# Performance work log

Hardware: AMD Instinct MI355X
Metric: run time of the kernel (lower is better)

The kernel has to match this reference:

```python
import jax, jax.numpy as jnp
import numpy as np
import math

B, S, D = 4, 2048, 1024
H, DH = 16, 64  # num_heads, head dim (hardcoded 64 in module)


def setup_inputs() -> dict:
    key = jax.random.key(0)
    ks = jax.random.split(key, 5)
    scale = 0.02
    return {
        "x": jax.random.normal(ks[0], (B, S, D), dtype=jnp.float32),
        "W_Q": jax.random.normal(ks[1], (D, H * DH), dtype=jnp.float32) * scale,
        "W_K": jax.random.normal(ks[2], (D, H * DH), dtype=jnp.float32) * scale,
        "W_V": jax.random.normal(ks[3], (D, H * DH), dtype=jnp.float32) * scale,
        "W_O": jax.random.normal(ks[4], (H * DH, D), dtype=jnp.float32) * scale,
        "ln_gamma": jnp.ones((D,), dtype=jnp.float32),
        "ln_beta": jnp.zeros((D,), dtype=jnp.float32),
    }


def reference(x, W_Q, W_K, W_V, W_O, ln_gamma, ln_beta):
    # QKV projections (bias=False Linear: x @ W)
    q = (x @ W_Q).reshape(B, S, H, DH).transpose(0, 2, 1, 3)  # [B,H,S,DH]
    k = (x @ W_K).reshape(B, S, H, DH).transpose(0, 2, 1, 3)
    v = (x @ W_V).reshape(B, S, H, DH).transpose(0, 2, 1, 3)

    # scaled scores with causal mask (upper triangle, diag=1 -> -1e7)
    scores = jnp.einsum("bhsd,bhtd->bhst", q, k) / math.sqrt(DH)  # [B,H,S,S]
    causal = jnp.triu(jnp.ones((S, S), dtype=bool), k=1)
    scores = jnp.where(causal, jnp.float32(-1e7), scores)
    attn = jax.nn.softmax(scores, axis=-1)
    ctx = jnp.einsum("bhst,bhtd->bhsd", attn, v)  # [B,H,S,DH]

    # merge heads, output proj, residual, LayerNorm
    out = ctx.transpose(0, 2, 1, 3).reshape(B, S, H * DH) @ W_O + x
    mu = jnp.mean(out, axis=-1, keepdims=True)
    var = jnp.mean((out - mu) ** 2, axis=-1, keepdims=True)
    out = (out - mu) * jax.lax.rsqrt(var + 1e-5) * ln_gamma + ln_beta
    return out
```

## Files before the change

kernel.cpp:

```cpp
#include <hip/hip_runtime.h>
#include <hip/hip_bf16.h>
#include <cstdint>
#include <cstddef>

#define S_ 2048
#define D_ 1024
#define H_ 16
#define DH_ 64
#define M_ 8192

using bf16 = __bf16;
using bf16x4 = __attribute__((ext_vector_type(4))) __bf16;
using bf16x8 = __attribute__((ext_vector_type(8))) __bf16;
using f32x4 = __attribute__((ext_vector_type(4))) float;
using s16x4 = __attribute__((ext_vector_type(4))) short;

__device__ __forceinline__ void g2lds16(const bf16* g, bf16* l) {
  __builtin_amdgcn_global_load_lds(
      (const __attribute__((address_space(1))) void*)g,
      (__attribute__((address_space(3))) void*)l, 16, 0, 0);
}

__device__ __forceinline__ f32x4 mfma16(bf16x4 a, bf16x4 b, f32x4 c) {
#if __has_builtin(__builtin_amdgcn_mfma_f32_16x16x16_bf16)
  return __builtin_amdgcn_mfma_f32_16x16x16_bf16(a, b, c, 0, 0, 0);
#elif __has_builtin(__builtin_amdgcn_mfma_f32_16x16x16bf16_1k)
  return __builtin_amdgcn_mfma_f32_16x16x16bf16_1k(
      __builtin_bit_cast(s16x4, a), __builtin_bit_cast(s16x4, b), c, 0, 0, 0);
#else
  f32x4 d;
  asm("v_mfma_f32_16x16x16_bf16 %0, %1, %2, %3"
      : "=v"(d)
      : "v"(a), "v"(b), "v"(c));
  return d;
#endif
}

__global__ __launch_bounds__(256) void cvt_all_kernel(
    const float* __restrict__ x, const float* __restrict__ w0,
    const float* __restrict__ w1, const float* __restrict__ w2,
    const float* __restrict__ w3, bf16* __restrict__ xb,
    bf16* __restrict__ o0, bf16* __restrict__ o1, bf16* __restrict__ o2,
    bf16* __restrict__ o3) {
  __shared__ float tile[32][33];
  int bx = blockIdx.x;
  int tid = threadIdx.x;
  if (bx < 4096) {
    size_t i = ((size_t)bx * 256 + tid) * 8;
    float4 a = *(const float4*)(x + i);
    float4 b = *(const float4*)(x + i + 4);
    bf16x8 o;
    o[0] = (bf16)a.x; o[1] = (bf16)a.y; o[2] = (bf16)a.z; o[3] = (bf16)a.w;
    o[4] = (bf16)b.x; o[5] = (bf16)b.y; o[6] = (bf16)b.z; o[7] = (bf16)b.w;
    *(bf16x8*)(xb + i) = o;
    return;
  }
  int wb = bx - 4096;
  int wsel = wb >> 10; wb &= 1023;
  const float* W; bf16* O;
  switch (wsel) {
    case 0: W = w0; O = o0; break;
    case 1: W = w1; O = o1; break;
    case 2: W = w2; O = o2; break;
    default: W = w3; O = o3; break;
  }
  int n0 = (wb & 31) * 32;
  int k0 = (wb >> 5) * 32;
#pragma unroll
  for (int i = 0; i < 4; ++i) {
    int e = tid + i * 256; int rr = e >> 5, cc = e & 31;
    tile[rr][cc] = W[(size_t)(k0 + rr) * 1024 + n0 + cc];
  }
  __syncthreads();
#pragma unroll
  for (int i = 0; i < 4; ++i) {
    int e = tid + i * 256; int rr = e >> 5, cc = e & 31;
    O[(size_t)(n0 + rr) * 1024 + k0 + cc] = (bf16)tile[cc][rr];
  }
}

template <int MODE>
__global__ __launch_bounds__(512, 4) void gemm_kernel(
    const bf16* __restrict__ A,
    const bf16* __restrict__ Bt0, const bf16* __restrict__ Bt1,
    const bf16* __restrict__ Bt2,
    bf16* __restrict__ Qo, bf16* __restrict__ Ko, bf16* __restrict__ Vto,
    const float* __restrict__ xres, float* __restrict__ out) {
  extern __shared__ float4 smem4[];
  bf16* smem = (bf16*)smem4;

  constexpr int NWG = (MODE == 0) ? 768 : 256;
  constexpr int CPX = NWG / 8;
  constexpr int NBN = (MODE == 0) ? 12 : 4;
  const int wg = ((int)blockIdx.x & 7) * CPX + ((int)blockIdx.x >> 3);
  const int bn = wg % NBN, bm = wg / NBN;

  const bf16* Bt;
  int n0full = 0, wsel = 0;
  if constexpr (MODE == 0) {
    wsel = bn >> 2;
    Bt = (wsel == 0) ? Bt0 : (wsel == 1 ? Bt1 : Bt2);
    n0full = (bn & 3) * 256;
  } else {
    Bt = Bt0;
    n0full = bn * 256;
  }

  const int tid = threadIdx.x;
  const int wave = tid >> 6, lane = tid & 63;
  const int quad = lane >> 4, r = lane & 15;
  const int wm = (wave >> 2) * 64, wn = (wave & 3) * 64;

  const int lrow = lane >> 2;
  const int lcol = ((lane & 3) ^ (lrow & 3)) * 8;
  const int am = bm * 128 + wave * 16 + lrow;
  const bf16 *pA, *pB1, *pB2;
  if constexpr (MODE == 0) {
    pA = A + (size_t)am * 1024 + lcol;
  } else {
    pA = A + (size_t)(am >> 11) * (16 * (size_t)S_ * DH_) +
         (size_t)(am & 2047) * 64 + lcol;
  }
  const int bnr = n0full + wave * 16 + lrow;
  pB1 = Bt + (size_t)bnr * 1024 + lcol;
  pB2 = Bt + (size_t)(bnr + 128) * 1024 + lcol;
  constexpr ptrdiff_t dSum = (MODE == 0) ? 64 : (ptrdiff_t)S_ * DH_;
  ptrdiff_t dTog = 32;

  const int oA = wave * 512;
  const int oB1 = 4096 + wave * 512;
  const int oB2 = 8192 + wave * 512;

  auto stage = [&](bf16* base) {
    g2lds16(pA, base + oA);
    g2lds16(pB1, base + oB1);
    g2lds16(pB2, base + oB2);
    pA += dTog; dTog = dSum - dTog;
    pB1 += 32; pB2 += 32;
  };

  f32x4 acc[4][4];
  const f32x4 zero = {0.f, 0.f, 0.f, 0.f};
#pragma unroll
  for (int i = 0; i < 4; ++i)
#pragma unroll
    for (int j = 0; j < 4; ++j) acc[i][j] = zero;

  const int x0 = (quad ^ (r & 3)) * 8;
  const int raB = (wm + r) * 32;
  const int rbB = (wn + r) * 32;

  auto phase = [&](const bf16* buf) {
    const bf16* bA = buf;
    const bf16* bB = buf + 4096;
    bf16x8 af[4], bg[4];
#pragma unroll
    for (int i = 0; i < 4; ++i)
      af[i] = *(const bf16x8*)(bA + raB + i * 512 + x0);
#pragma unroll
    for (int j = 0; j < 4; ++j)
      bg[j] = *(const bf16x8*)(bB + rbB + j * 512 + x0);
    __builtin_amdgcn_s_setprio(1);
#pragma unroll
    for (int i = 0; i < 4; ++i)
#pragma unroll
      for (int j = 0; j < 4; ++j)
        acc[i][j] = __builtin_amdgcn_mfma_f32_16x16x32_bf16(af[i], bg[j],
                                                            acc[i][j], 0, 0, 0);
    __builtin_amdgcn_s_setprio(0);
  };

  bf16* b0 = smem;
  bf16* b1 = smem + 12288;
  bf16* b2 = smem + 24576;

  stage(b0);
  stage(b1);

#pragma unroll 1
  for (int kt = 0; kt < 30; kt += 3) {
    asm volatile("s_waitcnt vmcnt(3)\n\ts_barrier" ::: "memory");
    stage(b2);
    phase(b0);
    asm volatile("s_waitcnt vmcnt(3)\n\ts_barrier" ::: "memory");
    stage(b0);
    phase(b1);
    asm volatile("s_waitcnt vmcnt(3)\n\ts_barrier" ::: "memory");
    stage(b1);
    phase(b2);
  }
  asm volatile("s_waitcnt vmcnt(3)\n\ts_barrier" ::: "memory");
  phase(b0);
  asm volatile("s_waitcnt vmcnt(0)\n\ts_barrier" ::: "memory");
  phase(b1);

  const int mB = bm * 128 + wm + quad * 4;
  if constexpr (MODE == 0) {
    if (wsel < 2) {
      bf16* dst = (wsel == 0) ? Qo : Ko;
#pragma unroll
      for (int i = 0; i < 4; ++i) {
#pragma unroll
        for (int j = 0; j < 4; ++j) {
          int n = n0full + wn + j * 16 + r;
          int h = n >> 6, dh = n & 63;
#pragma unroll
          for (int g = 0; g < 4; ++g) {
            int m = mB + i * 16 + g;
            int b = m >> 11, s = m & 2047;
            dst[((size_t)(b * H_ + h) * S_ + s) * DH_ + dh] =
                (bf16)acc[i][j][g];
          }
        }
      }
    } else {
#pragma unroll
      for (int i = 0; i < 4; ++i) {
        int m = mB + i * 16;
        int b = m >> 11, s = m & 2047;
#pragma unroll
        for (int j = 0; j < 4; ++j) {
          int n = n0full + wn + j * 16 + r;
          int h = n >> 6, dh = n & 63;
          bf16x4 pk;
#pragma unroll
          for (int g = 0; g < 4; ++g) pk[g] = (bf16)acc[i][j][g];
          *(bf16x4*)(Vto + ((size_t)(b * H_ + h) * DH_ + dh) * S_ + s) = pk;
        }
      }
    }
  } else {
#pragma unroll
    for (int i = 0; i < 4; ++i) {
#pragma unroll
      for (int j = 0; j < 4; ++j) {
        int n = bn * 256 + wn + j * 16 + r;
#pragma unroll
        for (int g = 0; g < 4; ++g) {
          int m = mB + i * 16 + g;
          size_t idx = (size_t)m * 1024 + n;
          out[idx] = acc[i][j][g] + xres[idx];
        }
      }
    }
  }
}

__global__ __launch_bounds__(512, 4) void attn_kernel(const bf16* __restrict__ Qb,
                                                      const bf16* __restrict__ Kb,
                                                      const bf16* __restrict__ Vtb,
                                                      bf16* __restrict__ ctx) {
  __shared__ __align__(16) bf16 smK[2][2][64 * 64];
  __shared__ __align__(16) bf16 smV[2][2][64 * 64];
  const int bx = blockIdx.x;
  const int bh = bx & 63;
  const int i256 = (bx < 256) ? (7 - (bx >> 6)) : ((bx - 256) >> 6);
  const bf16* Qh = Qb + (size_t)bh * S_ * DH_;
  const bf16* Kh = Kb + (size_t)bh * S_ * DH_;
  const bf16* Vh = Vtb + (size_t)bh * DH_ * S_;
  bf16* Ch = ctx + (size_t)bh * S_ * DH_;
  const int tid = threadIdx.x, wave = tid >> 6, lane = tid & 63;
  const int quad = lane >> 4, r = lane & 15;
  const int r7 = r & 7;
  const int wrow = wave * 8 + (lane >> 3);
  const int gcol = ((lane & 7) ^ (lane >> 3)) * 8;
  const f32x4 zero = {0.f, 0.f, 0.f, 0.f};
  const int xk0 = (quad ^ r7) * 8, xk1 = ((quad + 4) ^ r7) * 8;

  const int q0w = i256 * 256 + wave * 32;
  const int numkt = 4 * i256 + 4;
  const int NU = numkt >> 1;
  const int lastkt = q0w >> 6;

  bf16x8 qf[2][2];
  const float qsc = 0.125f * 1.44269504f;
#pragma unroll
  for (int qg = 0; qg < 2; ++qg)
#pragma unroll
    for (int hh = 0; hh < 2; ++hh) {
      bf16x8 q = *(const bf16x8*)(Qh + (size_t)(q0w + qg * 16 + r) * DH_ +
                                  hh * 32 + quad * 8);
#pragma unroll
      for (int i = 0; i < 8; ++i) q[i] = (bf16)((float)q[i] * qsc);
      qf[qg][hh] = q;
    }

  f32x4 lacc[2] = {zero, zero};
  f32x4 oacc[2][4];
#pragma unroll
  for (int qg = 0; qg < 2; ++qg)
#pragma unroll
    for (int tn = 0; tn < 4; ++tn) oacc[qg][tn] = zero;

  auto STAGE = [&](int u, int b) {
#pragma unroll
    for (int sub = 0; sub < 2; ++sub) {
      const int kt = 2 * u + sub;
      g2lds16(Kh + (size_t)(kt * 64 + wrow) * DH_ + gcol,
              &smK[b][sub][wave * 512]);
      g2lds16(Vh + (size_t)wrow * S_ + kt * 64 + gcol,
              &smV[b][sub][wave * 512]);
    }
  };

  STAGE(0, 0);
  asm volatile("s_waitcnt vmcnt(0)\n\ts_barrier" ::: "memory");

#pragma unroll 1
  for (int u = 0; u < NU; ++u) {
    const int b = u & 1;
    if (u + 1 < NU) STAGE(u + 1, b ^ 1);
#pragma unroll
    for (int sub = 0; sub < 2; ++sub) {
      const int kt = 2 * u + sub;
      if (kt <= lastkt) {
        const int kv0 = kt * 64;
        const bf16* kb = &smK[b][sub][0];
        const bf16* vb = &smV[b][sub][0];

        f32x4 s[2][4];
#pragma unroll
        for (int t = 0; t < 4; ++t) {
          bf16x8 kf0 = *(const bf16x8*)(kb + (t * 16 + r) * 64 + xk0);
          bf16x8 kf1 = *(const bf16x8*)(kb + (t * 16 + r) * 64 + xk1);
#pragma unroll
          for (int qg = 0; qg < 2; ++qg) {
            f32x4 z = __builtin_amdgcn_mfma_f32_16x16x32_bf16(kf0, qf[qg][0],
                                                              zero, 0, 0, 0);
            s[qg][t] = __builtin_amdgcn_mfma_f32_16x16x32_bf16(kf1, qf[qg][1],
                                                               z, 0, 0, 0);
          }
        }
        if (kt == lastkt) {
#pragma unroll
          for (int qg = 0; qg < 2; ++qg) {
            const int q = q0w + qg * 16 + r;
#pragma unroll
            for (int t = 0; t < 4; ++t) {
              const int kv = kv0 + t * 16 + quad * 4;
#pragma unroll
              for (int g = 0; g < 4; ++g)
                if (kv + g > q) s[qg][t][g] = -1e30f;
            }
          }
        }
#pragma unroll
        for (int t = 0; t < 4; ++t) {
          bf16x4 pa[2];
#pragma unroll
          for (int qg = 0; qg < 2; ++qg) {
#pragma unroll
            for (int g = 0; g < 4; ++g)
              s[qg][t][g] = __builtin_amdgcn_exp2f(s[qg][t][g]);
            lacc[qg] += s[qg][t];
            bf16x4 pk;
#pragma unroll
            for (int g = 0; g < 4; ++g) pk[g] = (bf16)s[qg][t][g];
            pa[qg] = pk;
          }
#pragma unroll
          for (int tn = 0; tn < 4; ++tn) {
            bf16x4 vf = *(const bf16x4*)(
                vb + (tn * 16 + r) * 64 +
                ((2 * t + (quad >> 1)) ^ r7) * 8 + (quad & 1) * 4);
            oacc[0][tn] = mfma16(pa[0], vf, oacc[0][tn]);
            oacc[1][tn] = mfma16(pa[1], vf, oacc[1][tn]);
          }
        }
      }
    }
    asm volatile("s_waitcnt vmcnt(0) lgkmcnt(0)\n\ts_barrier" ::: "memory");
  }

#pragma unroll
  for (int qg = 0; qg < 2; ++qg) {
    float rs = (lacc[qg][0] + lacc[qg][1]) + (lacc[qg][2] + lacc[qg][3]);
    rs += __shfl_xor(rs, 16, 64);
    rs += __shfl_xor(rs, 32, 64);
    const float inv = 1.f / rs;
    f32x4 ib;
#pragma unroll
    for (int g = 0; g < 4; ++g) ib[g] = __shfl(inv, quad * 4 + g, 64);
#pragma unroll
    for (int tn = 0; tn < 4; ++tn) {
      f32x4 ov = oacc[qg][tn] * ib;
#pragma unroll
      for (int g = 0; g < 4; ++g)
        Ch[(size_t)(q0w + qg * 16 + quad * 4 + g) * DH_ + tn * 16 + r] =
            (bf16)ov[g];
    }
  }
}

__global__ __launch_bounds__(256) void ln_kernel(float* __restrict__ out,
                                                 const float* __restrict__ gamma,
                                                 const float* __restrict__ beta) {
  __shared__ float red[8];
  size_t row = blockIdx.x;
  float* p = out + row * 1024;
  int tid = threadIdx.x;
  float4 v = ((const float4*)p)[tid];
  float s1 = v.x + v.y + v.z + v.w;
  float s2 = v.x * v.x + v.y * v.y + v.z * v.z + v.w * v.w;
#pragma unroll
  for (int o = 1; o < 64; o <<= 1) {
    s1 += __shfl_xor(s1, o, 64);
    s2 += __shfl_xor(s2, o, 64);
  }
  int wave = tid >> 6, lane = tid & 63;
  if (lane == 0) { red[wave] = s1; red[4 + wave] = s2; }
  __syncthreads();
  s1 = red[0] + red[1] + red[2] + red[3];
  s2 = red[4] + red[5] + red[6] + red[7];
  float mean = s1 * (1.f / 1024.f);
  float var = s2 * (1.f / 1024.f) - mean * mean;
  float rstd = rsqrtf(var + 1e-5f);
  float4 g = ((const float4*)gamma)[tid];
  float4 b = ((const float4*)beta)[tid];
  float4 o;
  o.x = (v.x - mean) * rstd * g.x + b.x;
  o.y = (v.y - mean) * rstd * g.y + b.y;
  o.z = (v.z - mean) * rstd * g.z + b.z;
  o.w = (v.w - mean) * rstd * g.w + b.w;
  ((float4*)p)[tid] = o;
}

extern "C" void kernel_launch(void* const* d_in, const int* in_sizes, int n_in,
                              void* d_out, int out_size, void* d_ws,
                              size_t ws_size, hipStream_t stream) {
  (void)in_sizes; (void)n_in; (void)out_size; (void)ws_size;
  const float* x  = (const float*)d_in[0];
  const float* WQ = (const float*)d_in[1];
  const float* WK = (const float*)d_in[2];
  const float* WV = (const float*)d_in[3];
  const float* WO = (const float*)d_in[4];
  const float* gamma = (const float*)d_in[5];
  const float* beta  = (const float*)d_in[6];
  float* out = (float*)d_out;

  bf16* ws = (bf16*)d_ws;
  const size_t MD = (size_t)M_ * D_;
  const size_t WW = (size_t)D_ * D_;
  bf16* xb   = ws;
  bf16* wqt  = xb + MD;
  bf16* wkt  = wqt + WW;
  bf16* wvt  = wkt + WW;
  bf16* wot  = wvt + WW;
  bf16* Qb   = wot + WW;
  bf16* Kb   = Qb + MD;
  bf16* Vtb  = Kb + MD;
  bf16* ctxb = Vtb + MD;

  constexpr int GEMM_LDS = 3 * 24 * 1024;
  static bool s_attr = false;
  if (!s_attr) {
    s_attr = true;
    (void)hipFuncSetAttribute(reinterpret_cast<const void*>(gemm_kernel<0>),
                              hipFuncAttributeMaxDynamicSharedMemorySize,
                              GEMM_LDS);
    (void)hipFuncSetAttribute(reinterpret_cast<const void*>(gemm_kernel<1>),
                              hipFuncAttributeMaxDynamicSharedMemorySize,
                              GEMM_LDS);
  }

  cvt_all_kernel<<<dim3(8192), dim3(256), 0, stream>>>(
      x, WQ, WK, WV, WO, xb, wqt, wkt, wvt, wot);
  gemm_kernel<0><<<dim3(768), dim3(512), GEMM_LDS, stream>>>(
      xb, wqt, wkt, wvt, Qb, Kb, Vtb, nullptr, nullptr);
  attn_kernel<<<dim3(512), dim3(512), 0, stream>>>(Qb, Kb, Vtb, ctxb);
  gemm_kernel<1><<<dim3(256), dim3(512), GEMM_LDS, stream>>>(
      ctxb, wot, nullptr, nullptr, nullptr, nullptr, nullptr, x, out);
  ln_kernel<<<dim3(8192), dim3(256), 0, stream>>>(out, gamma, beta);
}
```

Measured before the change: 248.7 us.

## Replace QKV projection GEMM with 256x256-tile double-buffered LDS pipeline kernel

Adds a dedicated QKV projection kernel that computes 256x256 output tiles per workgroup (384 workgroups instead of 768), using 128KB of LDS split into double buffers for A and B. Global-to-LDS direct loads are interleaved with 16x16x32 bf16 MFMA phases under manual waitcnt/barrier scheduling and setprio. The goal is more operand reuse per LDS byte and better overlap of memory traffic with compute. In exchange it uses a large LDS footprint that limits occupancy to about one workgroup per CU, and the hand-scheduled waitcnt counts are fragile.

```diff
diff --git a/kernel.cpp b/kernel.cpp
--- a/kernel.cpp
+++ b/kernel.cpp
@@ -76,6 +76,182 @@
   for (int i = 0; i < 4; ++i) {
     int e = tid + i * 256; int rr = e >> 5, cc = e & 31;
     O[(size_t)(n0 + rr) * 1024 + k0 + cc] = (bf16)tile[cc][rr];
+  }
+}
+
+__global__ __launch_bounds__(512, 2) void gemm256_kernel(
+    const bf16* __restrict__ A, const bf16* __restrict__ Bt0,
+    const bf16* __restrict__ Bt1, const bf16* __restrict__ Bt2,
+    bf16* __restrict__ Qo, bf16* __restrict__ Ko, bf16* __restrict__ Vto) {
+  extern __shared__ float4 smem4[];
+  bf16* smA = (bf16*)smem4;
+  bf16* smB = smA + 32768;
+
+  const int wg = ((int)blockIdx.x & 7) * 48 + ((int)blockIdx.x >> 3);
+  const int bn = wg % 12, bm = wg / 12;
+  const int wsel = bn >> 2;
+  const bf16* Bt = (wsel == 0) ? Bt0 : (wsel == 1 ? Bt1 : Bt2);
+  const int n0 = (bn & 3) * 256;
+
+  const int tid = threadIdx.x;
+  const int wave = tid >> 6, lane = tid & 63;
+  const int quad = lane >> 4, r = lane & 15;
+  const int wr = wave >> 2, wc = wave & 3;
+
+  const int srow = lane >> 3;
+  const int scol = ((lane & 7) ^ srow) * 8;
+  const int rbase = wave * 16;
+
+  const int gA = bm * 256;
+  const bf16 *pA00 = A + (size_t)(gA + rbase + srow) * 1024 + scol;
+  const bf16 *pA01 = A + (size_t)(gA + rbase + 8 + srow) * 1024 + scol;
+  const bf16 *pA10 = A + (size_t)(gA + 128 + rbase + srow) * 1024 + scol;
+  const bf16 *pA11 = A + (size_t)(gA + 128 + rbase + 8 + srow) * 1024 + scol;
+  const bf16 *pB00 = Bt + (size_t)(n0 + rbase + srow) * 1024 + scol;
+  const bf16 *pB01 = Bt + (size_t)(n0 + rbase + 8 + srow) * 1024 + scol;
+  const bf16 *pB10 = Bt + (size_t)(n0 + 128 + rbase + srow) * 1024 + scol;
+  const bf16 *pB11 = Bt + (size_t)(n0 + 128 + rbase + 8 + srow) * 1024 + scol;
+
+  auto stA_h0 = [&](bf16* b) {
+    g2lds16(pA00, b + rbase * 64); pA00 += 64;
+    g2lds16(pA01, b + (rbase + 8) * 64); pA01 += 64;
+  };
+  auto stA_h1 = [&](bf16* b) {
+    g2lds16(pA10, b + (128 + rbase) * 64); pA10 += 64;
+    g2lds16(pA11, b + (128 + rbase + 8) * 64); pA11 += 64;
+  };
+  auto stB_h0 = [&](bf16* b) {
+    g2lds16(pB00, b + rbase * 64); pB00 += 64;
+    g2lds16(pB01, b + (rbase + 8) * 64); pB01 += 64;
+  };
+  auto stB_h1 = [&](bf16* b) {
+    g2lds16(pB10, b + (128 + rbase) * 64); pB10 += 64;
+    g2lds16(pB11, b + (128 + rbase + 8) * 64); pB11 += 64;
+  };
+
+  f32x4 acc[8][4];
+  const f32x4 zero = {0.f, 0.f, 0.f, 0.f};
+#pragma unroll
+  for (int i = 0; i < 8; ++i)
+#pragma unroll
+    for (int j = 0; j < 4; ++j) acc[i][j] = zero;
+
+  const int x0 = (quad ^ (r & 7)) * 8;
+  const int x1 = ((quad + 4) ^ (r & 7)) * 8;
+  const int raB = (wr * 128 + r) * 64;
+  const int rbB = (wc * 64 + r) * 64;
+
+  bf16x8 af[4], bg[4];
+  auto LDA = [&](const bf16* bA, int fb, int xk) {
+#pragma unroll
+    for (int ii = 0; ii < 4; ++ii)
+      af[ii] = *(const bf16x8*)(bA + raB + (fb + ii) * 1024 + xk);
+  };
+  auto LDB = [&](const bf16* bB, int xk) {
+#pragma unroll
+    for (int j = 0; j < 4; ++j)
+      bg[j] = *(const bf16x8*)(bB + rbB + j * 1024 + xk);
+  };
+  auto MM = [&](int base) {
+    __builtin_amdgcn_s_setprio(1);
+#pragma unroll
+    for (int ii = 0; ii < 4; ++ii)
+#pragma unroll
+      for (int j = 0; j < 4; ++j)
+        acc[base + ii][j] = __builtin_amdgcn_mfma_f32_16x16x32_bf16(
+            af[ii], bg[j], acc[base + ii][j], 0, 0, 0);
+    __builtin_amdgcn_s_setprio(0);
+  };
+
+  bf16* bA0 = smA;          bf16* bA1 = smA + 16384;
+  bf16* bB0 = smB;          bf16* bB1 = smB + 16384;
+
+  stB_h0(bB0); stB_h1(bB0); stA_h0(bA0); stA_h1(bA0); stB_h0(bB1);
+
+#pragma unroll 1
+  for (int it = 0; it < 7; ++it) {
+    asm volatile("s_waitcnt vmcnt(4)\n\ts_barrier" ::: "memory");
+    LDA(bA0, 0, x0); LDB(bB0, x0);
+    stB_h1(bB1);
+    MM(0);
+    asm volatile("s_barrier" ::: "memory");
+    LDA(bA0, 4, x0);
+    stA_h0(bA1);
+    MM(4);
+    asm volatile("s_barrier" ::: "memory");
+    LDA(bA0, 0, x1); LDB(bB0, x1);
+    stA_h1(bA1);
+    MM(0);
+    asm volatile("s_barrier" ::: "memory");
+    LDA(bA0, 4, x1);
+    stB_h0(bB0);
+    MM(4);
+    asm volatile("s_waitcnt vmcnt(4)\n\ts_barrier" ::: "memory");
+    LDA(bA1, 0, x0); LDB(bB1, x0);
+    stB_h1(bB0);
+    MM(0);
+    asm volatile("s_barrier" ::: "memory");
+    LDA(bA1, 4, x0);
+    stA_h0(bA0);
+    MM(4);
+    asm volatile("s_barrier" ::: "memory");
+    LDA(bA1, 0, x1); LDB(bB1, x1);
+    stA_h1(bA0);
+    MM(0);
+    asm volatile("s_barrier" ::: "memory");
+    LDA(bA1, 4, x1);
+    stB_h0(bB1);
+    MM(4);
+  }
+  asm volatile("s_waitcnt vmcnt(4)\n\ts_barrier" ::: "memory");
+  LDA(bA0, 0, x0); LDB(bB0, x0); stB_h1(bB1); MM(0);
+  asm volatile("s_barrier" ::: "memory");
+  LDA(bA0, 4, x0); stA_h0(bA1); MM(4);
+  asm volatile("s_barrier" ::: "memory");
+  LDA(bA0, 0, x1); LDB(bB0, x1); stA_h1(bA1); MM(0);
+  asm volatile("s_barrier" ::: "memory");
+  LDA(bA0, 4, x1); MM(4);
+  asm volatile("s_waitcnt vmcnt(0)\n\ts_barrier" ::: "memory");
+  LDA(bA1, 0, x0); LDB(bB1, x0); MM(0);
+  asm volatile("s_barrier" ::: "memory");
+  LDA(bA1, 4, x0); MM(4);
+  asm volatile("s_barrier" ::: "memory");
+  LDA(bA1, 0, x1); LDB(bB1, x1); MM(0);
+  asm volatile("s_barrier" ::: "memory");
+  LDA(bA1, 4, x1); MM(4);
+
+  const int mB = bm * 256 + wr * 128 + quad * 4;
+  if (wsel < 2) {
+    bf16* dst = (wsel == 0) ? Qo : Ko;
+#pragma unroll
+    for (int i = 0; i < 8; ++i) {
+#pragma unroll
+      for (int j = 0; j < 4; ++j) {
+        int n = n0 + wc * 64 + j * 16 + r;
+        int h = n >> 6, dh = n & 63;
+#pragma unroll
+        for (int g = 0; g < 4; ++g) {
+          int m = mB + i * 16 + g;
+          int b = m >> 11, s = m & 2047;
+          dst[((size_t)(b * H_ + h) * S_ + s) * DH_ + dh] = (bf16)acc[i][j][g];
+        }
+      }
+    }
+  } else {
+#pragma unroll
+    for (int i = 0; i < 8; ++i) {
+      int m = mB + i * 16;
+      int b = m >> 11, s = m & 2047;
+#pragma unroll
+      for (int j = 0; j < 4; ++j) {
+        int n = n0 + wc * 64 + j * 16 + r;
+        int h = n >> 6, dh = n & 63;
+        bf16x4 pk;
+#pragma unroll
+        for (int g = 0; g < 4; ++g) pk[g] = (bf16)acc[i][j][g];
+        *(bf16x4*)(Vto + ((size_t)(b * H_ + h) * DH_ + dh) * S_ + s) = pk;
+      }
+    }
   }
 }
 
@@ -451,13 +627,14 @@
   bf16* Vtb  = Kb + MD;
   bf16* ctxb = Vtb + MD;
 
+  constexpr int G256_LDS = 128 * 1024;
   constexpr int GEMM_LDS = 3 * 24 * 1024;
   static bool s_attr = false;
   if (!s_attr) {
     s_attr = true;
-    (void)hipFuncSetAttribute(reinterpret_cast<const void*>(gemm_kernel<0>),
+    (void)hipFuncSetAttribute(reinterpret_cast<const void*>(gemm256_kernel),
                               hipFuncAttributeMaxDynamicSharedMemorySize,
-                              GEMM_LDS);
+                              G256_LDS);
     (void)hipFuncSetAttribute(reinterpret_cast<const void*>(gemm_kernel<1>),
                               hipFuncAttributeMaxDynamicSharedMemorySize,
                               GEMM_LDS);
@@ -465,8 +642,8 @@
 
   cvt_all_kernel<<<dim3(8192), dim3(256), 0, stream>>>(
       x, WQ, WK, WV, WO, xb, wqt, wkt, wvt, wot);
-  gemm_kernel<0><<<dim3(768), dim3(512), GEMM_LDS, stream>>>(
-      xb, wqt, wkt, wvt, Qb, Kb, Vtb, nullptr, nullptr);
+  gemm256_kernel<<<dim3(384), dim3(512), G256_LDS, stream>>>(
+      xb, wqt, wkt, wvt, Qb, Kb, Vtb);
   attn_kernel<<<dim3(512), dim3(512), 0, stream>>>(Qb, Kb, Vtb, ctxb);
   gemm_kernel<1><<<dim3(256), dim3(512), GEMM_LDS, stream>>>(
       ctxb, wot, nullptr, nullptr, nullptr, nullptr, nullptr, x, out);
```

Measured after the change: 247.4 us. Within noise of the previous version (-0.5%).
